# Kernel optimization log

Measured on AMD Instinct MI355X. Metric: run time of the kernel, lower is better.

Reference implementation:

```python
import jax, jax.numpy as jnp
import numpy as np

N_NODES = 50000
N_EDGES = 800000
D = 101
L = 2
NEG_SLOPE = 0.2


def setup_inputs() -> dict:
    key = jax.random.key(0)
    k1, k2, k3, k4, k5 = jax.random.split(key, 5)
    x = jax.random.normal(k1, (N_NODES, D), dtype=jnp.float32)
    edge_index = jax.random.randint(k2, (2, N_EDGES), 0, N_NODES, dtype=jnp.int64)
    # Glorot-ish scaled params, one set per layer
    Ws = jax.random.normal(k3, (L, D, D), dtype=jnp.float32) / np.sqrt(D)
    att_src = jax.random.normal(k4, (L, D), dtype=jnp.float32) / np.sqrt(D)
    att_dst = jax.random.normal(k5, (L, D), dtype=jnp.float32) / np.sqrt(D)
    bias = jnp.zeros((L, D), dtype=jnp.float32)
    return {"x": x, "edge_index": edge_index, "Ws": Ws,
            "att_src": att_src, "att_dst": att_dst, "bias": bias}


def _gat_layer(x, W, a_src, a_dst, b, src, dst):
    # x: [N, D]; src/dst: [E'] (self-loops included)
    h = x @ W                                   # [N, D]
    alpha_s = h @ a_src                         # [N]
    alpha_d = h @ a_dst                         # [N]
    e = alpha_s[src] + alpha_d[dst]             # [E']
    e = jnp.where(e > 0, e, NEG_SLOPE * e)      # leaky_relu
    # segment softmax over edges grouped by destination node
    m = jax.ops.segment_max(e, dst, num_segments=N_NODES)   # [N]
    w = jnp.exp(e - m[dst])                                 # [E']
    z = jax.ops.segment_sum(w, dst, num_segments=N_NODES)   # [N]
    coef = w / (z[dst] + 1e-16)                             # [E']
    out = jax.ops.segment_sum(h[src] * coef[:, None], dst,
                              num_segments=N_NODES)         # [N, D]
    return out + b


def reference(x, edge_index, Ws, att_src, att_dst, bias):
    # Add self-loops once (PyG GATConv default add_self_loops=True)
    loops = jnp.arange(N_NODES, dtype=edge_index.dtype)
    src = jnp.concatenate([edge_index[0], loops])
    dst = jnp.concatenate([edge_index[1], loops])
    for l in range(L):
        x = _gat_layer(x, Ws[l], att_src[l], att_dst[l], bias[l], src, dst)
    return x
```

## Files before the change

kernel.cpp:

```cpp
#include <hip/hip_runtime.h>
#include <math.h>

#define NN 50000
#define NE 800000
#define ET (NE + NN)
#define DF 101
#define HP 104
#define NEG 0.2f
#define MAXK 8
#define BM 32

__device__ __forceinline__ unsigned short f2bf(float f) {
    unsigned u = __float_as_uint(f);
    unsigned r = u + 0x7FFFu + ((u >> 16) & 1u);
    return (unsigned short)(r >> 16);
}
__device__ __forceinline__ float bflo(unsigned v) { return __uint_as_float(v << 16); }
__device__ __forceinline__ float bfhi(unsigned v) { return __uint_as_float(v & 0xFFFF0000u); }

__global__ __launch_bounds__(256) void proj_a(
    const float* __restrict__ W, const float* __restrict__ a_s,
    const float* __restrict__ a_d,
    float* __restrict__ wa_s, float* __restrict__ wa_d)
{
    int k = blockIdx.x * 4 + (threadIdx.x >> 6);
    if (k >= DF) return;
    int lane = threadIdx.x & 63;
    const float* wr = W + (size_t)k * DF;
    float w0 = wr[lane];
    float w1 = (lane < DF - 64) ? wr[64 + lane] : 0.f;
    float s1 = (lane < DF - 64) ? a_s[64 + lane] : 0.f;
    float d1 = (lane < DF - 64) ? a_d[64 + lane] : 0.f;
    float ps = w0 * a_s[lane] + w1 * s1;
    float pd = w0 * a_d[lane] + w1 * d1;
    #pragma unroll
    for (int off = 32; off; off >>= 1) {
        ps += __shfl_xor(ps, off);
        pd += __shfl_xor(pd, off);
    }
    if (lane == 0) { wa_s[k] = ps; wa_d[k] = pd; }
}

__global__ __launch_bounds__(256) void alpha_n(
    const float* __restrict__ x, const float* __restrict__ wa_s,
    const float* __restrict__ wa_d,
    float* __restrict__ as_n, float* __restrict__ ad_n)
{
    int n = blockIdx.x * 4 + (threadIdx.x >> 6);
    if (n >= NN) return;
    int lane = threadIdx.x & 63;
    const float* xr = x + (size_t)n * DF;
    float x0 = xr[lane];
    float x1v = (lane < DF - 64) ? xr[64 + lane] : 0.f;
    float s1  = (lane < DF - 64) ? wa_s[64 + lane] : 0.f;
    float d1  = (lane < DF - 64) ? wa_d[64 + lane] : 0.f;
    float ps = x0 * wa_s[lane] + x1v * s1;
    float pd = x0 * wa_d[lane] + x1v * d1;
    #pragma unroll
    for (int off = 32; off; off >>= 1) {
        ps += __shfl_xor(ps, off);
        pd += __shfl_xor(pd, off);
    }
    if (lane == 0) { as_n[n] = ps; ad_n[n] = pd; }
}

__global__ __launch_bounds__(256) void gemm_h(
    const float* __restrict__ x, const float* __restrict__ W,
    unsigned short* __restrict__ h16)
{
    __shared__ float xt[DF][BM + 4];
    const int t    = threadIdx.x;
    const int col  = t & 127;
    const int rg   = t >> 7;
    const int row0 = blockIdx.x * BM;

    if (t < DF) {
        #pragma unroll
        for (int r = 0; r < BM; ++r)
            xt[t][r] = (row0 + r < NN) ? x[(size_t)(row0 + r) * DF + t] : 0.f;
    }
    __syncthreads();

    float acc[16];
    #pragma unroll
    for (int r = 0; r < 16; ++r) acc[r] = 0.f;

    for (int k = 0; k < DF; ++k) {
        float wv = (col < DF) ? W[k * DF + col] : 0.f;
        const float4* xk = (const float4*)xt[k];
        #pragma unroll
        for (int j = 0; j < 4; ++j) {
            float4 xv = xk[rg * 4 + j];
            acc[j * 4 + 0] = fmaf(xv.x, wv, acc[j * 4 + 0]);
            acc[j * 4 + 1] = fmaf(xv.y, wv, acc[j * 4 + 1]);
            acc[j * 4 + 2] = fmaf(xv.z, wv, acc[j * 4 + 2]);
            acc[j * 4 + 3] = fmaf(xv.w, wv, acc[j * 4 + 3]);
        }
    }

    #pragma unroll
    for (int r = 0; r < 16; ++r) {
        int row = row0 + rg * 16 + r;
        if (row < NN) {
            if (col < DF)      h16[(size_t)row * HP + col] = f2bf(acc[r]);
            else if (col < HP) h16[(size_t)row * HP + col] = 0;
        }
    }
}


__global__ void count_deg(const int* __restrict__ ei, int* __restrict__ deg) {
    int i = blockIdx.x * blockDim.x + threadIdx.x;
    if (i >= ET) return;
    int d = (i < NE) ? ei[NE + i] : (i - NE);
    atomicAdd(&deg[d], 1);
}

__global__ __launch_bounds__(256) void scanA(const int* __restrict__ deg,
                                             int* __restrict__ part, int* __restrict__ aux) {
    __shared__ int sh[256];
    int t = threadIdx.x;
    int i = blockIdx.x * 256 + t;
    int v = (i < NN) ? deg[i] : 0;
    sh[t] = v; __syncthreads();
    #pragma unroll
    for (int off = 1; off < 256; off <<= 1) {
        int u = (t >= off) ? sh[t - off] : 0;
        __syncthreads();
        sh[t] += u;
        __syncthreads();
    }
    if (i < NN) part[i] = sh[t];
    if (t == 255) aux[blockIdx.x] = sh[255];
}

__global__ __launch_bounds__(256) void scanB(const int* __restrict__ aux,
                                             int* __restrict__ auxex, int nb) {
    __shared__ int sh[256];
    int t = threadIdx.x;
    int v = (t < nb) ? aux[t] : 0;
    sh[t] = v; __syncthreads();
    #pragma unroll
    for (int off = 1; off < 256; off <<= 1) {
        int u = (t >= off) ? sh[t - off] : 0;
        __syncthreads();
        sh[t] += u;
        __syncthreads();
    }
    if (t < nb) auxex[t] = sh[t] - v;
}

__global__ void scanC(const int* __restrict__ part, const int* __restrict__ auxex,
                      int* __restrict__ rowptr) {
    int i = blockIdx.x * blockDim.x + threadIdx.x;
    if (i == 0) rowptr[0] = 0;
    if (i < NN) rowptr[i + 1] = part[i] + auxex[i >> 8];
}

__global__ void scatter_edges(const int* __restrict__ ei, const int* __restrict__ rowptr,
                              int* __restrict__ cur, int* __restrict__ srclist) {
    int i = blockIdx.x * blockDim.x + threadIdx.x;
    if (i >= ET) return;
    int s, d;
    if (i < NE) { s = ei[i]; d = ei[NE + i]; } else { s = d = i - NE; }
    int pos = rowptr[d] + atomicAdd(&cur[d], 1);
    srclist[pos] = s;
}

__global__ __launch_bounds__(256) void gat_agg(
    const int* __restrict__ rowptr, const int* __restrict__ srclist,
    const float* __restrict__ a_s, const float* __restrict__ a_d,
    const unsigned short* __restrict__ h16, const float* __restrict__ bias,
    float* __restrict__ out)
{
    __shared__ __align__(16) uint2 ls[4][64];
    const int wv = threadIdx.x >> 6;
    int d = blockIdx.x * 4 + wv;
    if (d >= NN) return;
    int lane = threadIdx.x & 63;
    int s0 = rowptr[d], s1 = rowptr[d + 1];
    float ad = a_d[d];

    float earr[MAXK];
    int mysrc[MAXK];
    float mymax = -INFINITY;
    #pragma unroll
    for (int k = 0; k < MAXK; ++k) {
        int j = s0 + lane + k * 64;
        if (j < s1) {
            int s = srclist[j];
            mysrc[k] = s;
            float e = a_s[s] + ad;
            e = e > 0.f ? e : NEG * e;
            earr[k] = e;
            mymax = fmaxf(mymax, e);
        }
    }
    #pragma unroll
    for (int off = 32; off; off >>= 1)
        mymax = fmaxf(mymax, __shfl_xor(mymax, off));

    float sum = 0.f;
    #pragma unroll
    for (int k = 0; k < MAXK; ++k) {
        int j = s0 + lane + k * 64;
        if (j < s1) {
            float w = __expf(earr[k] - mymax);
            earr[k] = w;
            sum += w;
        }
    }
    #pragma unroll
    for (int off = 32; off; off >>= 1)
        sum += __shfl_xor(sum, off);
    float invz = 1.f / (sum + 1e-16f);

    const int li = (lane < 51) ? lane : 51;
    float acc0 = 0.f, acc1 = 0.f;
    #pragma unroll
    for (int k = 0; k < MAXK; ++k) {
        int jb = s0 + k * 64;
        if (jb >= s1) break;
        int lim = s1 - jb; if (lim > 64) lim = 64;
        ls[wv][lane] = make_uint2(__float_as_uint(earr[k] * invz),
                                  (unsigned)mysrc[k]);

        int i = 0;
        for (; i + 8 <= lim; i += 8) {
            uint4 q0 = *(const uint4*)&ls[wv][i];
            uint4 q1 = *(const uint4*)&ls[wv][i + 2];
            uint4 q2 = *(const uint4*)&ls[wv][i + 4];
            uint4 q3 = *(const uint4*)&ls[wv][i + 6];
            unsigned v0 = *((const unsigned*)(h16 + (size_t)q0.y * HP) + li);
            unsigned v1 = *((const unsigned*)(h16 + (size_t)q0.w * HP) + li);
            unsigned v2 = *((const unsigned*)(h16 + (size_t)q1.y * HP) + li);
            unsigned v3 = *((const unsigned*)(h16 + (size_t)q1.w * HP) + li);
            unsigned v4 = *((const unsigned*)(h16 + (size_t)q2.y * HP) + li);
            unsigned v5 = *((const unsigned*)(h16 + (size_t)q2.w * HP) + li);
            unsigned v6 = *((const unsigned*)(h16 + (size_t)q3.y * HP) + li);
            unsigned v7 = *((const unsigned*)(h16 + (size_t)q3.w * HP) + li);
            float c0 = __uint_as_float(q0.x), c1 = __uint_as_float(q0.z);
            float c2 = __uint_as_float(q1.x), c3 = __uint_as_float(q1.z);
            float c4 = __uint_as_float(q2.x), c5 = __uint_as_float(q2.z);
            float c6 = __uint_as_float(q3.x), c7 = __uint_as_float(q3.z);
            acc0 = fmaf(c0, bflo(v0), acc0); acc1 = fmaf(c0, bfhi(v0), acc1);
            acc0 = fmaf(c1, bflo(v1), acc0); acc1 = fmaf(c1, bfhi(v1), acc1);
            acc0 = fmaf(c2, bflo(v2), acc0); acc1 = fmaf(c2, bfhi(v2), acc1);
            acc0 = fmaf(c3, bflo(v3), acc0); acc1 = fmaf(c3, bfhi(v3), acc1);
            acc0 = fmaf(c4, bflo(v4), acc0); acc1 = fmaf(c4, bfhi(v4), acc1);
            acc0 = fmaf(c5, bflo(v5), acc0); acc1 = fmaf(c5, bfhi(v5), acc1);
            acc0 = fmaf(c6, bflo(v6), acc0); acc1 = fmaf(c6, bfhi(v6), acc1);
            acc0 = fmaf(c7, bflo(v7), acc0); acc1 = fmaf(c7, bfhi(v7), acc1);
        }
        for (; i + 4 <= lim; i += 4) {
            uint4 q0 = *(const uint4*)&ls[wv][i];
            uint4 q1 = *(const uint4*)&ls[wv][i + 2];
            unsigned v0 = *((const unsigned*)(h16 + (size_t)q0.y * HP) + li);
            unsigned v1 = *((const unsigned*)(h16 + (size_t)q0.w * HP) + li);
            unsigned v2 = *((const unsigned*)(h16 + (size_t)q1.y * HP) + li);
            unsigned v3 = *((const unsigned*)(h16 + (size_t)q1.w * HP) + li);
            float c0 = __uint_as_float(q0.x), c1 = __uint_as_float(q0.z);
            float c2 = __uint_as_float(q1.x), c3 = __uint_as_float(q1.z);
            acc0 = fmaf(c0, bflo(v0), acc0); acc1 = fmaf(c0, bfhi(v0), acc1);
            acc0 = fmaf(c1, bflo(v1), acc0); acc1 = fmaf(c1, bfhi(v1), acc1);
            acc0 = fmaf(c2, bflo(v2), acc0); acc1 = fmaf(c2, bfhi(v2), acc1);
            acc0 = fmaf(c3, bflo(v3), acc0); acc1 = fmaf(c3, bfhi(v3), acc1);
        }
        for (; i < lim; ++i) {
            uint2 p = ls[wv][i];
            unsigned v = *((const unsigned*)(h16 + (size_t)p.y * HP) + li);
            float c = __uint_as_float(p.x);
            acc0 = fmaf(c, bflo(v), acc0);
            acc1 = fmaf(c, bfhi(v), acc1);
        }
    }
    int c0 = 2 * lane;
    if (c0 < DF)     out[(size_t)d * DF + c0]     = acc0 + bias[c0];
    if (c0 + 1 < DF) out[(size_t)d * DF + c0 + 1] = acc1 + bias[c0 + 1];
}

static inline size_t alignup(size_t v) { return (v + 255) & ~size_t(255); }

extern "C" void kernel_launch(void* const* d_in, const int* in_sizes, int n_in,
                              void* d_out, int out_size, void* d_ws, size_t ws_size,
                              hipStream_t stream)
{
    const float* x    = (const float*)d_in[0];
    const int*   ei   = (const int*)  d_in[1];
    const float* Ws   = (const float*)d_in[2];
    const float* a_s  = (const float*)d_in[3];
    const float* a_d  = (const float*)d_in[4];
    const float* bias = (const float*)d_in[5];
    float* out = (float*)d_out;

    char* w = (char*)d_ws;
    unsigned short* h16 = (unsigned short*)w; w += alignup((size_t)NN * HP * 2);
    float* x1      = (float*)w; w += alignup((size_t)NN * DF * 4);
    int*   srclist = (int*)w;   w += alignup((size_t)ET * 4);
    float* as_n    = (float*)w; w += alignup((size_t)NN * 4);
    float* ad_n    = (float*)w; w += alignup((size_t)NN * 4);
    int*   deg     = (int*)w;   w += alignup((size_t)NN * 4);
    int*   part    = (int*)w;   w += alignup((size_t)NN * 4);
    int*   cur     = (int*)w;   w += alignup((size_t)NN * 4);
    int*   rowptr  = (int*)w;   w += alignup((size_t)(NN + 1) * 4);
    int*   aux     = (int*)w;   w += alignup(256 * 4);
    int*   auxex   = (int*)w;   w += alignup(256 * 4);
    float* wa_s    = (float*)w; w += alignup(DF * 4);
    float* wa_d    = (float*)w; w += alignup(DF * 4);

    const int NB = (NN + 255) / 256;

    hipMemsetAsync(deg, 0, (size_t)NN * 4, stream);
    hipMemsetAsync(cur, 0, (size_t)NN * 4, stream);
    count_deg<<<(ET + 255) / 256, 256, 0, stream>>>(ei, deg);
    scanA<<<NB, 256, 0, stream>>>(deg, part, aux);
    scanB<<<1, 256, 0, stream>>>(aux, auxex, NB);
    scanC<<<NB, 256, 0, stream>>>(part, auxex, rowptr);
    scatter_edges<<<(ET + 255) / 256, 256, 0, stream>>>(ei, rowptr, cur, srclist);

    for (int l = 0; l < 2; ++l) {
        const float* curx = (l == 0) ? x : x1;
        float*       nxt  = (l == 0) ? x1 : out;
        const float* Wl   = Ws + l * DF * DF;

        proj_a<<<(DF + 3) / 4, 256, 0, stream>>>(Wl, a_s + l * DF, a_d + l * DF,
                                                 wa_s, wa_d);
        alpha_n<<<(NN + 3) / 4, 256, 0, stream>>>(curx, wa_s, wa_d, as_n, ad_n);
        gemm_h<<<(NN + BM - 1) / BM, 256, 0, stream>>>(curx, Wl, h16);
        gat_agg<<<(NN + 3) / 4, 256, 0, stream>>>(rowptr, srclist, as_n, ad_n,
                                                  h16, bias + l * DF, nxt);
    }
}
```

Before: 352.8 us.

## Use bf16 MFMA for feature GEMM and record atomic ranks to skip second atomic pass

Replaces the scalar FP32 x@W GEMM with a bf16 MFMA 16x16x32 kernel. It pre-transposes and pads W to bf16 once per layer, and stages x tiles in LDS converted to bf16. It also records each edge's atomic rank during degree counting, so the scatter step writes positions directly without a second atomic pass or memset. Inputs to the GEMM are now rounded to bf16 rather than computed in FP32, which lowers accuracy, and a 16-bit rank buffer is added.

```diff
diff --git a/kernel.cpp b/kernel.cpp
--- a/kernel.cpp
+++ b/kernel.cpp
@@ -8,7 +8,14 @@
 #define HP 104
 #define NEG 0.2f
 #define MAXK 8
-#define BM 32
+
+#define GM 64
+#define KP 128
+#define NP 112
+#define LSTR 136
+
+typedef __attribute__((ext_vector_type(8))) short bf16x8;
+typedef __attribute__((ext_vector_type(4))) float f32x4;
 
 __device__ __forceinline__ unsigned short f2bf(float f) {
     unsigned u = __float_as_uint(f);
@@ -64,56 +71,75 @@
     if (lane == 0) { as_n[n] = ps; ad_n[n] = pd; }
 }
 
+__global__ void prep_wt(const float* __restrict__ W, unsigned short* __restrict__ wtb) {
+    int i = blockIdx.x * 256 + threadIdx.x;
+    if (i >= NP * KP) return;
+    int c = i >> 7;
+    int k = i & (KP - 1);
+    float v = (c < DF && k < DF) ? W[k * DF + c] : 0.f;
+    wtb[c * KP + k] = f2bf(v);
+}
+
 __global__ __launch_bounds__(256) void gemm_h(
-    const float* __restrict__ x, const float* __restrict__ W,
+    const float* __restrict__ x, const unsigned short* __restrict__ wtb,
     unsigned short* __restrict__ h16)
 {
-    __shared__ float xt[DF][BM + 4];
-    const int t    = threadIdx.x;
-    const int col  = t & 127;
-    const int rg   = t >> 7;
-    const int row0 = blockIdx.x * BM;
-
-    if (t < DF) {
+    __shared__ unsigned short xs[GM * LSTR];
+    __shared__ unsigned short ws[NP * LSTR];
+    const int t = threadIdx.x;
+    const int row0 = blockIdx.x * GM;
+
+    {
+        const uint4* src = (const uint4*)wtb;
+        for (int i = t; i < NP * 16; i += 256) {
+            int r = i >> 4, seg = i & 15;
+            uint4 v = src[r * 16 + seg];
+            *(uint4*)&ws[r * LSTR + seg * 8] = v;
+        }
+    }
+    for (int i = t; i < GM * KP; i += 256) {
+        int r = i >> 7, k = i & (KP - 1);
+        int row = row0 + r;
+        float v = (k < DF && row < NN) ? x[(size_t)row * DF + k] : 0.f;
+        xs[r * LSTR + k] = f2bf(v);
+    }
+    __syncthreads();
+
+    const int wv = t >> 6, lane = t & 63;
+    const int arow = wv * 16 + (lane & 15);
+    const int kgrp = (lane >> 4) * 8;
+
+    bf16x8 a[4];
+    #pragma unroll
+    for (int ks = 0; ks < 4; ++ks)
+        a[ks] = *(const bf16x8*)&xs[arow * LSTR + ks * 32 + kgrp];
+
+    #pragma unroll
+    for (int nt = 0; nt < 7; ++nt) {
+        f32x4 acc = {0.f, 0.f, 0.f, 0.f};
+        const int col = nt * 16 + (lane & 15);
         #pragma unroll
-        for (int r = 0; r < BM; ++r)
-            xt[t][r] = (row0 + r < NN) ? x[(size_t)(row0 + r) * DF + t] : 0.f;
-    }
-    __syncthreads();
-
-    float acc[16];
-    #pragma unroll
-    for (int r = 0; r < 16; ++r) acc[r] = 0.f;
-
-    for (int k = 0; k < DF; ++k) {
-        float wv = (col < DF) ? W[k * DF + col] : 0.f;
-        const float4* xk = (const float4*)xt[k];
+        for (int ks = 0; ks < 4; ++ks) {
+            bf16x8 b = *(const bf16x8*)&ws[col * LSTR + ks * 32 + kgrp];
+            acc = __builtin_amdgcn_mfma_f32_16x16x32_bf16(a[ks], b, acc, 0, 0, 0);
+        }
+        const int rbase = row0 + wv * 16 + (lane >> 4) * 4;
         #pragma unroll
-        for (int j = 0; j < 4; ++j) {
-            float4 xv = xk[rg * 4 + j];
-            acc[j * 4 + 0] = fmaf(xv.x, wv, acc[j * 4 + 0]);
-            acc[j * 4 + 1] = fmaf(xv.y, wv, acc[j * 4 + 1]);
-            acc[j * 4 + 2] = fmaf(xv.z, wv, acc[j * 4 + 2]);
-            acc[j * 4 + 3] = fmaf(xv.w, wv, acc[j * 4 + 3]);
-        }
-    }
-
-    #pragma unroll
-    for (int r = 0; r < 16; ++r) {
-        int row = row0 + rg * 16 + r;
-        if (row < NN) {
-            if (col < DF)      h16[(size_t)row * HP + col] = f2bf(acc[r]);
-            else if (col < HP) h16[(size_t)row * HP + col] = 0;
-        }
-    }
-}
-
-
-__global__ void count_deg(const int* __restrict__ ei, int* __restrict__ deg) {
+        for (int r = 0; r < 4; ++r) {
+            int row = rbase + r;
+            if (col < HP && row < NN)
+                h16[(size_t)row * HP + col] = f2bf(acc[r]);
+        }
+    }
+}
+
+
+__global__ void count_rank(const int* __restrict__ ei, int* __restrict__ deg,
+                           unsigned short* __restrict__ rank) {
     int i = blockIdx.x * blockDim.x + threadIdx.x;
     if (i >= ET) return;
     int d = (i < NE) ? ei[NE + i] : (i - NE);
-    atomicAdd(&deg[d], 1);
+    rank[i] = (unsigned short)atomicAdd(&deg[d], 1);
 }
 
 __global__ __launch_bounds__(256) void scanA(const int* __restrict__ deg,
@@ -157,14 +183,14 @@
     if (i < NN) rowptr[i + 1] = part[i] + auxex[i >> 8];
 }
 
-__global__ void scatter_edges(const int* __restrict__ ei, const int* __restrict__ rowptr,
-                              int* __restrict__ cur, int* __restrict__ srclist) {
+__global__ void scatter_plain(const int* __restrict__ ei, const int* __restrict__ rowptr,
+                              const unsigned short* __restrict__ rank,
+                              int* __restrict__ srclist) {
     int i = blockIdx.x * blockDim.x + threadIdx.x;
     if (i >= ET) return;
     int s, d;
     if (i < NE) { s = ei[i]; d = ei[NE + i]; } else { s = d = i - NE; }
-    int pos = rowptr[d] + atomicAdd(&cur[d], 1);
-    srclist[pos] = s;
+    srclist[rowptr[d] + rank[i]] = s;
 }
 
 __global__ __launch_bounds__(256) void gat_agg(
@@ -294,14 +320,16 @@
     float* out = (float*)d_out;
 
     char* w = (char*)d_ws;
-    unsigned short* h16 = (unsigned short*)w; w += alignup((size_t)NN * HP * 2);
+    unsigned short* h16  = (unsigned short*)w; w += alignup((size_t)NN * HP * 2);
     float* x1      = (float*)w; w += alignup((size_t)NN * DF * 4);
     int*   srclist = (int*)w;   w += alignup((size_t)ET * 4);
+    unsigned short* rank = (unsigned short*)w; w += alignup((size_t)ET * 2);
+    unsigned short* wtb0 = (unsigned short*)w; w += alignup((size_t)NP * KP * 2);
+    unsigned short* wtb1 = (unsigned short*)w; w += alignup((size_t)NP * KP * 2);
     float* as_n    = (float*)w; w += alignup((size_t)NN * 4);
     float* ad_n    = (float*)w; w += alignup((size_t)NN * 4);
     int*   deg     = (int*)w;   w += alignup((size_t)NN * 4);
     int*   part    = (int*)w;   w += alignup((size_t)NN * 4);
-    int*   cur     = (int*)w;   w += alignup((size_t)NN * 4);
     int*   rowptr  = (int*)w;   w += alignup((size_t)(NN + 1) * 4);
     int*   aux     = (int*)w;   w += alignup(256 * 4);
     int*   auxex   = (int*)w;   w += alignup(256 * 4);
@@ -309,24 +337,28 @@
     float* wa_d    = (float*)w; w += alignup(DF * 4);
 
     const int NB = (NN + 255) / 256;
+    const int NWT = (NP * KP + 255) / 256;
+
+    prep_wt<<<NWT, 256, 0, stream>>>(Ws,               wtb0);
+    prep_wt<<<NWT, 256, 0, stream>>>(Ws + DF * DF,     wtb1);
 
     hipMemsetAsync(deg, 0, (size_t)NN * 4, stream);
-    hipMemsetAsync(cur, 0, (size_t)NN * 4, stream);
-    count_deg<<<(ET + 255) / 256, 256, 0, stream>>>(ei, deg);
+    count_rank<<<(ET + 255) / 256, 256, 0, stream>>>(ei, deg, rank);
     scanA<<<NB, 256, 0, stream>>>(deg, part, aux);
     scanB<<<1, 256, 0, stream>>>(aux, auxex, NB);
     scanC<<<NB, 256, 0, stream>>>(part, auxex, rowptr);
-    scatter_edges<<<(ET + 255) / 256, 256, 0, stream>>>(ei, rowptr, cur, srclist);
+    scatter_plain<<<(ET + 255) / 256, 256, 0, stream>>>(ei, rowptr, rank, srclist);
 
     for (int l = 0; l < 2; ++l) {
         const float* curx = (l == 0) ? x : x1;
         float*       nxt  = (l == 0) ? x1 : out;
         const float* Wl   = Ws + l * DF * DF;
+        const unsigned short* wtb = (l == 0) ? wtb0 : wtb1;
 
         proj_a<<<(DF + 3) / 4, 256, 0, stream>>>(Wl, a_s + l * DF, a_d + l * DF,
                                                  wa_s, wa_d);
         alpha_n<<<(NN + 3) / 4, 256, 0, stream>>>(curx, wa_s, wa_d, as_n, ad_n);
-        gemm_h<<<(NN + BM - 1) / BM, 256, 0, stream>>>(curx, Wl, h16);
+        gemm_h<<<(NN + GM - 1) / GM, 256, 0, stream>>>(curx, wtb, h16);
         gat_agg<<<(NN + 3) / 4, 256, 0, stream>>>(rowptr, srclist, as_n, ad_n,
                                                   h16, bias + l * DF, nxt);
     }
```

After: 302.6 us. 14.2% less time.
